# Kernel tuning notes

Hardware: AMD Instinct MI355X
Metric: run time of the kernel (lower is better)

## Reference

```python
import jax, jax.numpy as jnp
import numpy as np

N_NODES = 100000


def _gcn_conv(x, W, b, src, dst, num_nodes):
    # PyG GCNConv: h = x @ W, symmetric norm deg^{-1/2} (self-loops already in src/dst),
    # out[i] = sum_{j->i} norm_ij * h[j] + b
    h = x @ W
    deg = jax.ops.segment_sum(jnp.ones_like(src, dtype=x.dtype), dst, num_segments=num_nodes)
    dinv = jnp.where(deg > 0, jax.lax.rsqrt(jnp.maximum(deg, 1.0)), 0.0)
    norm = dinv[src] * dinv[dst]  # [E]
    msg = h[src] * norm[:, None]  # gather + scale, [E, d]
    out = jax.ops.segment_sum(msg, dst, num_segments=num_nodes)
    return out + b


def setup_inputs() -> dict:
    key = jax.random.key(0)
    k1, k2, k3, k4 = jax.random.split(key, 4)
    d = 64
    E = 1600000
    x = jax.random.normal(k1, (N_NODES, d), dtype=jnp.float32)
    edge_index = jax.random.randint(k2, (2, E), 0, N_NODES, dtype=jnp.int64)
    W1 = jax.random.normal(k3, (d, d), dtype=jnp.float32) / np.sqrt(d)
    b1 = jnp.zeros((d,), dtype=jnp.float32)
    W2 = jax.random.normal(k4, (d, d), dtype=jnp.float32) / np.sqrt(d)
    b2 = jnp.zeros((d,), dtype=jnp.float32)
    return {"x": x, "edge_index": edge_index, "W1": W1, "b1": b1, "W2": W2, "b2": b2}


def reference(x, edge_index, W1, b1, W2, b2):
    num_nodes = x.shape[0]
    # add self loops once (shared by both convs)
    loops = jnp.arange(num_nodes, dtype=edge_index.dtype)
    src = jnp.concatenate([edge_index[0], loops])
    dst = jnp.concatenate([edge_index[1], loops])
    x1 = jax.nn.relu(_gcn_conv(x, W1, b1, src, dst, num_nodes))
    # dropout in eval mode == identity (deterministic reference)
    x2 = _gcn_conv(x1, W2, b2, src, dst, num_nodes)
    return x2 + x
```

## Files before the change

### kernel.cpp

```cpp
#include <hip/hip_runtime.h>
#include <hip/hip_bf16.h>

#define DFEAT 64
#define BNODES 128
#define BCAP 2560
#define EPB 8192

typedef __attribute__((ext_vector_type(8))) short short8;
typedef __attribute__((ext_vector_type(4))) float f32x4;

__device__ __forceinline__ unsigned short f2bf(float f) {
    unsigned u = __float_as_uint(f);
    return (unsigned short)((u + 0x7FFFu + ((u >> 16) & 1u)) >> 16);
}
__device__ __forceinline__ float bflo(unsigned u) { return __uint_as_float(u << 16); }
__device__ __forceinline__ float bfhi(unsigned u) { return __uint_as_float(u & 0xFFFF0000u); }


__global__ __launch_bounds__(256) void zero_cur_k(int* __restrict__ bcur, int n) {
    int i = blockIdx.x * 256 + threadIdx.x;
    if (i < n) bcur[i] = 0;
}

__global__ __launch_bounds__(256) void bucketize_k(const int* __restrict__ src,
                                                   const int* __restrict__ dst,
                                                   int* __restrict__ bcur,
                                                   unsigned* __restrict__ barr,
                                                   int E, int NB) {
    __shared__ unsigned pkbuf[EPB];
    __shared__ unsigned short bbuf[EPB];
    __shared__ int hist[784];
    __shared__ int base[784];

    int tid = threadIdx.x;
    int e0 = blockIdx.x * EPB;
    int n = min(EPB, E - e0);

    for (int t = tid; t < NB; t += 256) hist[t] = 0;
    __syncthreads();

    for (int k = 0; k < EPB / 256; ++k) {
        int i = k * 256 + tid;
        if (i < n) {
            int d = dst[e0 + i];
            int b = d >> 7;
            pkbuf[i] = ((unsigned)(d & 127) << 25) | (unsigned)src[e0 + i];
            bbuf[i] = (unsigned short)b;
            atomicAdd(&hist[b], 1);
        }
    }
    __syncthreads();

    for (int t = tid; t < NB; t += 256) {
        int c = hist[t];
        if (c > 0) base[t] = atomicAdd(&bcur[t], c);
        hist[t] = 0;
    }
    __syncthreads();

    for (int k = 0; k < EPB / 256; ++k) {
        int i = k * 256 + tid;
        if (i < n) {
            int b = bbuf[i];
            int loc = atomicAdd(&hist[b], 1);
            int pos = base[b] + loc;
            if (pos < BCAP) barr[(size_t)b * BCAP + pos] = pkbuf[i];
        }
    }
}

__global__ __launch_bounds__(256) void localsort_k(const int* __restrict__ bcur,
                                                   unsigned* __restrict__ barr,
                                                   int* __restrict__ meta,
                                                   float* __restrict__ dinv, int N) {
    __shared__ int cnt[BNODES];
    __shared__ int off[BNODES];
    __shared__ int cur[BNODES];
    __shared__ int sorted[BCAP];
    int b = blockIdx.x;
    int nb = min(bcur[b], BCAP);
    const unsigned* p = barr + (size_t)b * BCAP;
    if (threadIdx.x < BNODES) cnt[threadIdx.x] = 0;
    __syncthreads();
    for (int i = threadIdx.x; i < nb; i += 256) atomicAdd(&cnt[p[i] >> 25], 1);
    __syncthreads();
    if (threadIdx.x < BNODES) off[threadIdx.x] = cnt[threadIdx.x];
    __syncthreads();
    for (int d = 1; d < BNODES; d <<= 1) {
        int v = 0;
        if (threadIdx.x < BNODES && threadIdx.x >= d) v = off[threadIdx.x - d];
        __syncthreads();
        if (threadIdx.x < BNODES) off[threadIdx.x] += v;
        __syncthreads();
    }
    if (threadIdx.x < BNODES) {
        int ex = off[threadIdx.x] - cnt[threadIdx.x];
        cur[threadIdx.x] = ex;
        int node = b * BNODES + threadIdx.x;
        if (node < N) {
            meta[node] = (ex << 16) | cnt[threadIdx.x];
            dinv[node] = rsqrtf((float)cnt[threadIdx.x] + 1.0f);
        }
    }
    __syncthreads();
    for (int i = threadIdx.x; i < nb; i += 256) {
        unsigned w = p[i];
        int pos = atomicAdd(&cur[w >> 25], 1);
        sorted[pos] = (int)(w & 0x1FFFFFFu);
    }
    __syncthreads();
    int tot = off[BNODES - 1];
    for (int i = threadIdx.x; i < tot; i += 256)
        barr[(size_t)b * BCAP + i] = (unsigned)sorted[i];
}


__global__ __launch_bounds__(256) void prepW_k(const float* __restrict__ W1,
                                               const float* __restrict__ W2,
                                               unsigned short* __restrict__ W1f,
                                               unsigned short* __restrict__ W2f) {
    for (int idx = threadIdx.x; idx < 4096; idx += 256) {
        int j = idx & 7, lane = (idx >> 3) & 63, ct = (idx >> 9) & 3, kb = (idx >> 11) & 1;
        int k = kb * 32 + (lane >> 4) * 8 + j;
        int col = ct * 16 + (lane & 15);
        W1f[idx] = f2bf(W1[k * 64 + col]);
        W2f[idx] = f2bf(W2[k * 64 + col]);
    }
}

__global__ __launch_bounds__(256) void cvt_k(const float* __restrict__ x,
                                             unsigned short* __restrict__ Xb, int nq) {
    int i = blockIdx.x * 256 + threadIdx.x;
    if (i >= nq) return;
    float4 v = ((const float4*)x)[i];
    ushort4 r;
    r.x = f2bf(v.x); r.y = f2bf(v.y); r.z = f2bf(v.z); r.w = f2bf(v.w);
    ((ushort4*)Xb)[i] = r;
}


__global__ __launch_bounds__(256) void mgemm_k(const unsigned short* __restrict__ Xb,
                                               const unsigned short* __restrict__ Wf,
                                               const float* __restrict__ dinv,
                                               unsigned short* __restrict__ Ab,
                                               int ntile, int N) {
    int wv = threadIdx.x >> 6, l = threadIdx.x & 63;
    int tile = blockIdx.x * 4 + wv;
    if (tile >= ntile) return;
    int row0 = tile * 16;

    const short8* Xv = (const short8*)Xb;
    int ar = row0 + (l & 15);
    short8 a0 = Xv[ar * 8 + (l >> 4)];
    short8 a1 = Xv[ar * 8 + 4 + (l >> 4)];

    const short8* Wv = (const short8*)Wf;
    int rbase = row0 + (l >> 4) * 4;
    float dv0 = dinv[rbase + 0], dv1 = dinv[rbase + 1];
    float dv2 = dinv[rbase + 2], dv3 = dinv[rbase + 3];

#pragma unroll
    for (int ct = 0; ct < 4; ++ct) {
        f32x4 c = {0.0f, 0.0f, 0.0f, 0.0f};
        c = __builtin_amdgcn_mfma_f32_16x16x32_bf16(a0, Wv[ct * 64 + l], c, 0, 0, 0);
        c = __builtin_amdgcn_mfma_f32_16x16x32_bf16(a1, Wv[(4 + ct) * 64 + l], c, 0, 0, 0);
        int colb = ct * 16 + (l & 15);
        Ab[(size_t)(rbase + 0) * 64 + colb] = f2bf(c[0] * dv0);
        Ab[(size_t)(rbase + 1) * 64 + colb] = f2bf(c[1] * dv1);
        Ab[(size_t)(rbase + 2) * 64 + colb] = f2bf(c[2] * dv2);
        Ab[(size_t)(rbase + 3) * 64 + colb] = f2bf(c[3] * dv3);
    }
}


#define GATHER_BODY(EPILOGUE)                                                     \
    int lane = threadIdx.x & 31;                                                  \
    int node = blockIdx.x * 8 + (threadIdx.x >> 5);                               \
    if (node >= N) return;                                                        \
    int m = meta[node];                                                           \
    int cnt = m & 0xFFFF;                                                         \
    const int* lst = (const int*)ed + (size_t)(node >> 7) * BCAP + (m >> 16);     \
    unsigned su = Au[(size_t)node * 32 + lane];                                   \
    float ax = bflo(su), ay = bfhi(su);                            \
    int i = 0;                                                                    \
    for (; i + 4 <= cnt; i += 4) {                                                \
        int s0 = lst[i], s1 = lst[i + 1], s2 = lst[i + 2], s3 = lst[i + 3];       \
        unsigned u0 = Au[(size_t)s0 * 32 + lane];                                 \
        unsigned u1 = Au[(size_t)s1 * 32 + lane];                                 \
        unsigned u2 = Au[(size_t)s2 * 32 + lane];                                 \
        unsigned u3 = Au[(size_t)s3 * 32 + lane];                                 \
        ax += (bflo(u0) + bflo(u1)) + (bflo(u2) + bflo(u3));                      \
        ay += (bfhi(u0) + bfhi(u1)) + (bfhi(u2) + bfhi(u3));                      \
    }                                                                             \
    for (; i < cnt; ++i) {                                                        \
        unsigned u = Au[(size_t)lst[i] * 32 + lane];                              \
        ax += bflo(u);                                                            \
        ay += bfhi(u);                                                            \
    }                                                                             \
    float d = dinv[node];                                                         \
    float bx = bias[2 * lane], by = bias[2 * lane + 1];                           \
    EPILOGUE;

__global__ __launch_bounds__(256) void gat_relu_k(const int* __restrict__ meta,
                                                  const unsigned* __restrict__ ed,
                                                  const unsigned* __restrict__ Au,
                                                  const float* __restrict__ dinv,
                                                  const float* __restrict__ bias,
                                                  unsigned* __restrict__ xout, int N) {
    GATHER_BODY({
        float rx = fmaxf(fmaf(d, ax, bx), 0.0f);
        float ry = fmaxf(fmaf(d, ay, by), 0.0f);
        xout[(size_t)node * 32 + lane] = ((unsigned)f2bf(ry) << 16) | (unsigned)f2bf(rx);
    })
}

__global__ __launch_bounds__(256) void gat_res_k(const int* __restrict__ meta,
                                                 const unsigned* __restrict__ ed,
                                                 const unsigned* __restrict__ Au,
                                                 const float* __restrict__ dinv,
                                                 const float* __restrict__ bias,
                                                 const float* __restrict__ xres,
                                                 float* __restrict__ out, int N) {
    GATHER_BODY({
        float2 xr = ((const float2*)xres)[(size_t)node * 32 + lane];
        float2 r;
        r.x = fmaf(d, ax, bx + xr.x);
        r.y = fmaf(d, ay, by + xr.y);
        ((float2*)out)[(size_t)node * 32 + lane] = r;
    })
}


extern "C" void kernel_launch(void* const* d_in, const int* in_sizes, int n_in,
                              void* d_out, int out_size, void* d_ws, size_t ws_size,
                              hipStream_t stream) {
    const float* x = (const float*)d_in[0];
    const int* ei = (const int*)d_in[1];
    const float* W1 = (const float*)d_in[2];
    const float* b1 = (const float*)d_in[3];
    const float* W2 = (const float*)d_in[4];
    const float* b2 = (const float*)d_in[5];
    float* out = (float*)d_out;

    const int N = in_sizes[0] / DFEAT;
    const int E = in_sizes[1] / 2;
    const int NB = (N + BNODES - 1) / BNODES;
    const int NT = (N + 15) / 16;

    const int* src = ei;
    const int* dst = ei + E;

    char* w = (char*)d_ws;
    size_t o = 0;
    unsigned short* Xb = (unsigned short*)(w + o); o += (size_t)N * DFEAT * 2;
    unsigned short* Ab = (unsigned short*)(w + o); o += (size_t)N * DFEAT * 2;
    float* dinv = (float*)(w + o);                 o += ((size_t)N * 4 + 255) & ~255;
    int* meta = (int*)(w + o);                     o += ((size_t)N * 4 + 255) & ~255;
    int* bcur = (int*)(w + o);                     o += ((size_t)NB * 4 + 255) & ~255;
    unsigned short* W1f = (unsigned short*)(w + o); o += 4096 * 2;
    unsigned short* W2f = (unsigned short*)(w + o); o += 4096 * 2;
    o = (o + 255) & ~255;
    unsigned* barr = (unsigned*)(w + o);

    const int gB = (E + EPB - 1) / EPB;
    const int gG = (N + 7) / 8;
    const int gM = (NT + 3) / 4;

    zero_cur_k<<<(NB + 255) / 256, 256, 0, stream>>>(bcur, NB);
    bucketize_k<<<gB, 256, 0, stream>>>(src, dst, bcur, barr, E, NB);
    localsort_k<<<NB, 256, 0, stream>>>(bcur, barr, meta, dinv, N);
    cvt_k<<<(N * DFEAT / 4 + 255) / 256, 256, 0, stream>>>(x, Xb, N * DFEAT / 4);
    prepW_k<<<1, 256, 0, stream>>>(W1, W2, W1f, W2f);

    mgemm_k<<<gM, 256, 0, stream>>>(Xb, W1f, dinv, Ab, NT, N);
    gat_relu_k<<<gG, 256, 0, stream>>>(meta, barr, (const unsigned*)Ab, dinv, b1,
                                       (unsigned*)Xb, N);

    mgemm_k<<<gM, 256, 0, stream>>>(Xb, W2f, dinv, Ab, NT, N);
    gat_res_k<<<gG, 256, 0, stream>>>(meta, barr, (const unsigned*)Ab, dinv, b2, x, out, N);
}
```

Baseline: 158.8 us.

## Fuse fp32-to-bf16 conversion into GEMM and widen gather loads to 16 bytes

Drops the separate x-to-bf16 conversion kernel and has the first GEMM read fp32 x directly, converting to bf16 in registers. The gather kernels now split each 32-lane node group into four edge sub-groups of eight lanes, each lane loading a 16-byte uint4 of a neighbour row. Partial sums are combined with cross-lane shuffles. This raises bytes per load and edges in flight, at the cost of more registers and shuffle reductions. Edges per bucketize block also shrink from 8192 to 2048 to give that kernel more blocks.

```diff
diff --git a/kernel.cpp b/kernel.cpp
--- a/kernel.cpp
+++ b/kernel.cpp
@@ -4,7 +4,7 @@
 #define DFEAT 64
 #define BNODES 128
 #define BCAP 2560
-#define EPB 8192
+#define EPB 2048
 
 typedef __attribute__((ext_vector_type(8))) short short8;
 typedef __attribute__((ext_vector_type(4))) float f32x4;
@@ -128,18 +128,9 @@
     }
 }
 
-__global__ __launch_bounds__(256) void cvt_k(const float* __restrict__ x,
-                                             unsigned short* __restrict__ Xb, int nq) {
-    int i = blockIdx.x * 256 + threadIdx.x;
-    if (i >= nq) return;
-    float4 v = ((const float4*)x)[i];
-    ushort4 r;
-    r.x = f2bf(v.x); r.y = f2bf(v.y); r.z = f2bf(v.z); r.w = f2bf(v.w);
-    ((ushort4*)Xb)[i] = r;
-}
-
-
-__global__ __launch_bounds__(256) void mgemm_k(const unsigned short* __restrict__ Xb,
+
+template <bool F32IN>
+__global__ __launch_bounds__(256) void mgemm_k(const void* __restrict__ Xin,
                                                const unsigned short* __restrict__ Wf,
                                                const float* __restrict__ dinv,
                                                unsigned short* __restrict__ Ab,
@@ -148,11 +139,24 @@
     int tile = blockIdx.x * 4 + wv;
     if (tile >= ntile) return;
     int row0 = tile * 16;
-
-    const short8* Xv = (const short8*)Xb;
     int ar = row0 + (l & 15);
-    short8 a0 = Xv[ar * 8 + (l >> 4)];
-    short8 a1 = Xv[ar * 8 + 4 + (l >> 4)];
+
+    short8 a0, a1;
+    if constexpr (F32IN) {
+        const float* Xf = (const float*)Xin;
+        const float4* q = (const float4*)(Xf + (size_t)ar * 64 + (l >> 4) * 8);
+        float4 f0 = q[0], f1 = q[1];
+        const float4* q2 = (const float4*)(Xf + (size_t)ar * 64 + 32 + (l >> 4) * 8);
+        float4 g0 = q2[0], g1 = q2[1];
+        a0[0]=(short)f2bf(f0.x); a0[1]=(short)f2bf(f0.y); a0[2]=(short)f2bf(f0.z); a0[3]=(short)f2bf(f0.w);
+        a0[4]=(short)f2bf(f1.x); a0[5]=(short)f2bf(f1.y); a0[6]=(short)f2bf(f1.z); a0[7]=(short)f2bf(f1.w);
+        a1[0]=(short)f2bf(g0.x); a1[1]=(short)f2bf(g0.y); a1[2]=(short)f2bf(g0.z); a1[3]=(short)f2bf(g0.w);
+        a1[4]=(short)f2bf(g1.x); a1[5]=(short)f2bf(g1.y); a1[6]=(short)f2bf(g1.z); a1[7]=(short)f2bf(g1.w);
+    } else {
+        const short8* Xv = (const short8*)Xin;
+        a0 = Xv[ar * 8 + (l >> 4)];
+        a1 = Xv[ar * 8 + 4 + (l >> 4)];
+    }
 
     const short8* Wv = (const short8*)Wf;
     int rbase = row0 + (l >> 4) * 4;
@@ -173,61 +177,101 @@
 }
 
 
-#define GATHER_BODY(EPILOGUE)                                                     \
-    int lane = threadIdx.x & 31;                                                  \
-    int node = blockIdx.x * 8 + (threadIdx.x >> 5);                               \
-    if (node >= N) return;                                                        \
-    int m = meta[node];                                                           \
-    int cnt = m & 0xFFFF;                                                         \
-    const int* lst = (const int*)ed + (size_t)(node >> 7) * BCAP + (m >> 16);     \
-    unsigned su = Au[(size_t)node * 32 + lane];                                   \
-    float ax = bflo(su), ay = bfhi(su);                            \
-    int i = 0;                                                                    \
-    for (; i + 4 <= cnt; i += 4) {                                                \
-        int s0 = lst[i], s1 = lst[i + 1], s2 = lst[i + 2], s3 = lst[i + 3];       \
-        unsigned u0 = Au[(size_t)s0 * 32 + lane];                                 \
-        unsigned u1 = Au[(size_t)s1 * 32 + lane];                                 \
-        unsigned u2 = Au[(size_t)s2 * 32 + lane];                                 \
-        unsigned u3 = Au[(size_t)s3 * 32 + lane];                                 \
-        ax += (bflo(u0) + bflo(u1)) + (bflo(u2) + bflo(u3));                      \
-        ay += (bfhi(u0) + bfhi(u1)) + (bfhi(u2) + bfhi(u3));                      \
-    }                                                                             \
-    for (; i < cnt; ++i) {                                                        \
-        unsigned u = Au[(size_t)lst[i] * 32 + lane];                              \
-        ax += bflo(u);                                                            \
-        ay += bfhi(u);                                                            \
-    }                                                                             \
-    float d = dinv[node];                                                         \
-    float bx = bias[2 * lane], by = bias[2 * lane + 1];                           \
-    EPILOGUE;
+#define GATHER_BODY(...)                                                            \
+    int tid = threadIdx.x;                                                          \
+    int lane = tid & 31;                                                            \
+    int g = lane >> 3;                                         \
+    int sl = lane & 7;                                         \
+    int node = blockIdx.x * 8 + (tid >> 5);                                         \
+    if (node >= N) return;                                                          \
+    int m = meta[node];                                                             \
+    int cnt = m & 0xFFFF;                                                           \
+    const int* lst = (const int*)ed + (size_t)(node >> 7) * BCAP + (m >> 16);       \
+    const uint4* A4 = (const uint4*)Au;                                             \
+    float a0 = 0, a1 = 0, a2 = 0, a3 = 0, a4 = 0, a5 = 0, a6 = 0, a7 = 0;           \
+    if (g == 0) {                                                    \
+        uint4 su = A4[(size_t)node * 8 + sl];                                       \
+        a0 = bflo(su.x); a1 = bfhi(su.x); a2 = bflo(su.y); a3 = bfhi(su.y);         \
+        a4 = bflo(su.z); a5 = bfhi(su.z); a6 = bflo(su.w); a7 = bfhi(su.w);         \
+    }                                                                               \
+    int i = 0;                                                                      \
+    for (; i + 8 <= cnt; i += 8) {                                                  \
+        int sA = lst[i + g];                                                        \
+        int sB = lst[i + 4 + g];                                                    \
+        uint4 uA = A4[(size_t)sA * 8 + sl];                                         \
+        uint4 uB = A4[(size_t)sB * 8 + sl];                                         \
+        a0 += bflo(uA.x) + bflo(uB.x); a1 += bfhi(uA.x) + bfhi(uB.x);               \
+        a2 += bflo(uA.y) + bflo(uB.y); a3 += bfhi(uA.y) + bfhi(uB.y);               \
+        a4 += bflo(uA.z) + bflo(uB.z); a5 += bfhi(uA.z) + bfhi(uB.z);               \
+        a6 += bflo(uA.w) + bflo(uB.w); a7 += bfhi(uA.w) + bfhi(uB.w);               \
+    }                                                                               \
+    for (; i < cnt; i += 4) {                                                       \
+        int e = min(i + g, cnt - 1);                                                \
+        int s = lst[e];                                                             \
+        uint4 u = A4[(size_t)s * 8 + sl];                                           \
+        if (i + g >= cnt) { u.x = 0; u.y = 0; u.z = 0; u.w = 0; }                   \
+        a0 += bflo(u.x); a1 += bfhi(u.x); a2 += bflo(u.y); a3 += bfhi(u.y);         \
+        a4 += bflo(u.z); a5 += bfhi(u.z); a6 += bflo(u.w); a7 += bfhi(u.w);         \
+    }                                                                               \
+    a0 += __shfl_xor(a0, 8);  a1 += __shfl_xor(a1, 8);                              \
+    a2 += __shfl_xor(a2, 8);  a3 += __shfl_xor(a3, 8);                              \
+    a4 += __shfl_xor(a4, 8);  a5 += __shfl_xor(a5, 8);                              \
+    a6 += __shfl_xor(a6, 8);  a7 += __shfl_xor(a7, 8);                              \
+    a0 += __shfl_xor(a0, 16); a1 += __shfl_xor(a1, 16);                             \
+    a2 += __shfl_xor(a2, 16); a3 += __shfl_xor(a3, 16);                             \
+    a4 += __shfl_xor(a4, 16); a5 += __shfl_xor(a5, 16);                             \
+    a6 += __shfl_xor(a6, 16); a7 += __shfl_xor(a7, 16);                             \
+    if (g == 0) {                                                                   \
+        float d = dinv[node];                                                       \
+        float4 b0 = *(const float4*)(bias + sl * 8);                                \
+        float4 b1 = *(const float4*)(bias + sl * 8 + 4);                            \
+        __VA_ARGS__                                                                 \
+    }
 
 __global__ __launch_bounds__(256) void gat_relu_k(const int* __restrict__ meta,
                                                   const unsigned* __restrict__ ed,
-                                                  const unsigned* __restrict__ Au,
+                                                  const unsigned short* __restrict__ Au,
                                                   const float* __restrict__ dinv,
                                                   const float* __restrict__ bias,
                                                   unsigned* __restrict__ xout, int N) {
-    GATHER_BODY({
-        float rx = fmaxf(fmaf(d, ax, bx), 0.0f);
-        float ry = fmaxf(fmaf(d, ay, by), 0.0f);
-        xout[(size_t)node * 32 + lane] = ((unsigned)f2bf(ry) << 16) | (unsigned)f2bf(rx);
-    })
+    GATHER_BODY(
+        float r0 = fmaxf(fmaf(d, a0, b0.x), 0.0f);
+        float r1 = fmaxf(fmaf(d, a1, b0.y), 0.0f);
+        float r2 = fmaxf(fmaf(d, a2, b0.z), 0.0f);
+        float r3 = fmaxf(fmaf(d, a3, b0.w), 0.0f);
+        float r4 = fmaxf(fmaf(d, a4, b1.x), 0.0f);
+        float r5 = fmaxf(fmaf(d, a5, b1.y), 0.0f);
+        float r6 = fmaxf(fmaf(d, a6, b1.z), 0.0f);
+        float r7 = fmaxf(fmaf(d, a7, b1.w), 0.0f);
+        uint4 pk;
+        pk.x = ((unsigned)f2bf(r1) << 16) | f2bf(r0);
+        pk.y = ((unsigned)f2bf(r3) << 16) | f2bf(r2);
+        pk.z = ((unsigned)f2bf(r5) << 16) | f2bf(r4);
+        pk.w = ((unsigned)f2bf(r7) << 16) | f2bf(r6);
+        ((uint4*)xout)[(size_t)node * 8 + sl] = pk;
+    )
 }
 
 __global__ __launch_bounds__(256) void gat_res_k(const int* __restrict__ meta,
                                                  const unsigned* __restrict__ ed,
-                                                 const unsigned* __restrict__ Au,
+                                                 const unsigned short* __restrict__ Au,
                                                  const float* __restrict__ dinv,
                                                  const float* __restrict__ bias,
                                                  const float* __restrict__ xres,
                                                  float* __restrict__ out, int N) {
-    GATHER_BODY({
-        float2 xr = ((const float2*)xres)[(size_t)node * 32 + lane];
-        float2 r;
-        r.x = fmaf(d, ax, bx + xr.x);
-        r.y = fmaf(d, ay, by + xr.y);
-        ((float2*)out)[(size_t)node * 32 + lane] = r;
-    })
+    GATHER_BODY(
+        const float4* xq = (const float4*)(xres + (size_t)node * 64 + sl * 8);
+        float4 x0 = xq[0];
+        float4 x1 = xq[1];
+        float4 r0;
+        float4 r1;
+        r0.x = fmaf(d, a0, b0.x + x0.x); r0.y = fmaf(d, a1, b0.y + x0.y);
+        r0.z = fmaf(d, a2, b0.z + x0.z); r0.w = fmaf(d, a3, b0.w + x0.w);
+        r1.x = fmaf(d, a4, b1.x + x1.x); r1.y = fmaf(d, a5, b1.y + x1.y);
+        r1.z = fmaf(d, a6, b1.z + x1.z); r1.w = fmaf(d, a7, b1.w + x1.w);
+        float4* oq = (float4*)(out + (size_t)node * 64 + sl * 8);
+        oq[0] = r0; oq[1] = r1;
+    )
 }
 
 
@@ -269,13 +313,11 @@
     zero_cur_k<<<(NB + 255) / 256, 256, 0, stream>>>(bcur, NB);
     bucketize_k<<<gB, 256, 0, stream>>>(src, dst, bcur, barr, E, NB);
     localsort_k<<<NB, 256, 0, stream>>>(bcur, barr, meta, dinv, N);
-    cvt_k<<<(N * DFEAT / 4 + 255) / 256, 256, 0, stream>>>(x, Xb, N * DFEAT / 4);
     prepW_k<<<1, 256, 0, stream>>>(W1, W2, W1f, W2f);
 
-    mgemm_k<<<gM, 256, 0, stream>>>(Xb, W1f, dinv, Ab, NT, N);
-    gat_relu_k<<<gG, 256, 0, stream>>>(meta, barr, (const unsigned*)Ab, dinv, b1,
-                                       (unsigned*)Xb, N);
-
-    mgemm_k<<<gM, 256, 0, stream>>>(Xb, W2f, dinv, Ab, NT, N);
-    gat_res_k<<<gG, 256, 0, stream>>>(meta, barr, (const unsigned*)Ab, dinv, b2, x, out, N);
-}
+    mgemm_k<true><<<gM, 256, 0, stream>>>(x, W1f, dinv, Ab, NT, N);
+    gat_relu_k<<<gG, 256, 0, stream>>>(meta, barr, Ab, dinv, b1, (unsigned*)Xb, N);
+
+    mgemm_k<false><<<gM, 256, 0, stream>>>(Xb, W2f, dinv, Ab, NT, N);
+    gat_res_k<<<gG, 256, 0, stream>>>(meta, barr, Ab, dinv, b2, x, out, N);
+}
```

Result: faster. 149.2 us (-6.0%).
